# Kernel optimization log

Hardware: AMD Instinct MI355X
Metric: run time of the kernel (lower is better)

## Reference

```python
import jax, jax.numpy as jnp
import numpy as np

B, C, H, W = 4, 320, 32, 32
HEADS = 8
LTXT, DCROSS = 77, 768
HW = H * W


def _ln(x, w, b, eps=1e-5):
    mu = x.mean(-1, keepdims=True)
    var = jnp.var(x, axis=-1, keepdims=True)
    return (x - mu) * jax.lax.rsqrt(var + eps) * w + b


def _gn(x, w, b, groups=32, eps=1e-6):
    Bx, Cx, Hx, Wx = x.shape
    xg = x.reshape(Bx, groups, -1)
    mu = xg.mean(-1, keepdims=True)
    var = jnp.var(xg, axis=-1, keepdims=True)
    xn = ((xg - mu) * jax.lax.rsqrt(var + eps)).reshape(Bx, Cx, Hx, Wx)
    return xn * w[None, :, None, None] + b[None, :, None, None]


def _attn(q, k, v, bias=None):
    Bq, S, Cd = q.shape
    dh = Cd // HEADS
    qh = q.reshape(Bq, S, HEADS, dh)
    kh = k.reshape(Bq, -1, HEADS, dh)
    vh = v.reshape(Bq, -1, HEADS, dh)
    s = jnp.einsum('bqhd,bkhd->bhqk', qh, kh) * (1.0 / np.sqrt(dh))
    if bias is not None:
        s = s + bias  # additive 0/1 otsu mask, exactly as the torch code passes it
    p = jax.nn.softmax(s, axis=-1)
    o = jnp.einsum('bhqk,bkhd->bqhd', p, vh).reshape(Bq, S, Cd)
    return o, p


def _block(x, ctx, prm, bias=None):
    # BasicTransformerBlock: self-attn -> cross-attn (returns probs) -> GEGLU FF
    (ln1w, ln1b, qkv, ow, ob, ln2w, ln2b, q2, kv2, o2w, o2b,
     ln3w, ln3b, ff1w, ff1b, ff2w, ff2b) = prm
    h = _ln(x, ln1w, ln1b)
    q, k, v = jnp.split(h @ qkv, 3, axis=-1)
    o, _ = _attn(q, k, v)
    x = x + o @ ow + ob
    h = _ln(x, ln2w, ln2b)
    k2, v2 = jnp.split(ctx @ kv2, 2, axis=-1)
    o2, p2 = _attn(h @ q2, k2, v2, bias)
    x = x + o2 @ o2w + o2b
    h = _ln(x, ln3w, ln3b)
    a, g = jnp.split(h @ ff1w + ff1b, 2, axis=-1)
    x = x + (a * jax.nn.gelu(g)) @ ff2w + ff2b
    return x, p2


def _otsu(m):
    # vectorized version of the 10-threshold otsu loop (m: [B/2, N])
    mn = m.min(-1, keepdims=True)
    mx = m.max(-1, keepdims=True)
    x = (m - mn) / (mx - mn)
    n = x.shape[-1]
    ts = jnp.arange(10, dtype=x.dtype) * 0.1  # thresholds t*0.1
    low = x[:, None, :] < ts[None, :, None]   # [B/2, 10, N]
    cnt_low = low.sum(-1).astype(x.dtype)
    cnt_high = n - cnt_low
    sum_low = jnp.where(low, x[:, None, :], 0.0).sum(-1)
    sum_high = x.sum(-1, keepdims=True) - sum_low
    mu_low = jnp.where(cnt_low > 0, sum_low / jnp.maximum(cnt_low, 1.0), jnp.nan)
    mu_high = jnp.where(cnt_high > 0, sum_high / jnp.maximum(cnt_high, 1.0), jnp.nan)
    g = (cnt_low / n) * (cnt_high / n) * (mu_low - mu_high) ** 2
    g = jnp.where(jnp.isnan(g), -jnp.inf, g)  # torch: nan > max_g is False -> skipped
    best = jnp.argmax(g, axis=-1)             # first max == torch strict-> ties keep earliest
    gmax = jnp.take_along_axis(g, best[:, None], axis=-1)[:, 0]
    thr = jnp.where(gmax > 0, best.astype(x.dtype) * 0.1, 0.0)[:, None]
    return jnp.where(x < thr, 0.0, jnp.where(x > thr, 1.0, x))


def _fwd(gn_w, gn_b, pin_w, pin_b,
         b_ln1w, b_ln1b, b_qkv, b_ow, b_ob, b_ln2w, b_ln2b, b_q2, b_kv2, b_o2w, b_o2b,
         b_ln3w, b_ln3b, b_ff1w, b_ff1b, b_ff2w, b_ff2b,
         i_ln1w, i_ln1b, i_qkv, i_ow, i_ob, i_ln2w, i_ln2b, i_q2, i_kv2, i_o2w, i_o2b,
         i_ln3w, i_ln3b, i_ff1w, i_ff1b, i_ff2w, i_ff2b,
         pout_w, pout_b, hidden_states, encoder_hidden_states,
         ph_b, ph_t, eot_b, eot_t):
    residual = hidden_states
    h = _gn(hidden_states, gn_w, gn_b)
    h = h.transpose(0, 2, 3, 1).reshape(B, HW, C)
    h = h @ pin_w + pin_b  # use_linear_projection path
    blk = (b_ln1w, b_ln1b, b_qkv, b_ow, b_ob, b_ln2w, b_ln2b, b_q2, b_kv2, b_o2w, b_o2b,
           b_ln3w, b_ln3b, b_ff1w, b_ff1b, b_ff2w, b_ff2b)
    iblk = (i_ln1w, i_ln1b, i_qkv, i_ow, i_ob, i_ln2w, i_ln2b, i_q2, i_kv2, i_o2w, i_o2b,
            i_ln3w, i_ln3b, i_ff1w, i_ff1b, i_ff2w, i_ff2b)
    h, probs = _block(h, encoder_hidden_states, blk)   # probs [B, heads, HW, 77]
    ap = probs.mean(1)[B // 2:]                        # head-avg attn_probs, cond half
    attn = ap.transpose(0, 2, 1)                       # [B/2, 77, HW]
    attn_ph = attn[ph_b, ph_t]                         # [B/2, HW]
    attn_eot = jax.lax.stop_gradient(attn[eot_b, eot_t])
    loss_reg = jnp.mean((attn_ph / attn_ph.max(-1, keepdims=True)
                         - attn_eot / attn_eot.max(-1, keepdims=True)) ** 2)
    mask = _otsu(jax.lax.stop_gradient(attn_ph))       # [B/2, HW]
    bias = mask[:, None, None, :]                      # broadcast over heads and queries
    hs, img = h[:B // 2], h[B // 2:]
    hs, _ = _block(hs, img, iblk, bias)                # image_cross_attention
    h = jnp.concatenate([hs, img], axis=0)
    h = h @ pout_w + pout_b
    sample = h.reshape(B, H, W, C).transpose(0, 3, 1, 2) + residual
    return sample, loss_reg


def setup_inputs():
    key = jax.random.key(0)
    ki = iter(jax.random.split(key, 80))
    f32 = jnp.float32

    def rn(shape, s=0.02):
        return jax.random.normal(next(ki), shape, f32) * s

    def blk(p, cross):
        return {p + 'ln1w': jnp.ones((C,), f32), p + 'ln1b': jnp.zeros((C,), f32),
                p + 'qkv': rn((C, 3 * C)), p + 'ow': rn((C, C)), p + 'ob': jnp.zeros((C,), f32),
                p + 'ln2w': jnp.ones((C,), f32), p + 'ln2b': jnp.zeros((C,), f32),
                p + 'q2': rn((C, C)), p + 'kv2': rn((cross, 2 * C)),
                p + 'o2w': rn((C, C)), p + 'o2b': jnp.zeros((C,), f32),
                p + 'ln3w': jnp.ones((C,), f32), p + 'ln3b': jnp.zeros((C,), f32),
                p + 'ff1w': rn((C, 8 * C)), p + 'ff1b': jnp.zeros((8 * C,), f32),
                p + 'ff2w': rn((4 * C, C)), p + 'ff2b': jnp.zeros((C,), f32)}

    inp = {'gn_w': jnp.ones((C,), f32), 'gn_b': jnp.zeros((C,), f32),
           'pin_w': rn((C, C)), 'pin_b': jnp.zeros((C,), f32)}
    inp.update(blk('b_', DCROSS))
    inp.update(blk('i_', C))
    inp['pout_w'] = rn((C, C))
    inp['pout_b'] = jnp.zeros((C,), f32)
    inp['hidden_states'] = jax.random.normal(next(ki), (B, C, H, W), f32)
    inp['encoder_hidden_states'] = jax.random.normal(next(ki), (B, LTXT, DCROSS), f32)
    inp['ph_b'] = jnp.arange(B // 2)
    inp['ph_t'] = jax.random.randint(next(ki), (B // 2,), 0, LTXT)
    inp['eot_b'] = jnp.arange(B // 2)
    inp['eot_t'] = jax.random.randint(next(ki), (B // 2,), 0, LTXT)
    return inp


def reference(gn_w, gn_b, pin_w, pin_b,
              b_ln1w, b_ln1b, b_qkv, b_ow, b_ob, b_ln2w, b_ln2b, b_q2, b_kv2, b_o2w, b_o2b,
              b_ln3w, b_ln3b, b_ff1w, b_ff1b, b_ff2w, b_ff2b,
              i_ln1w, i_ln1b, i_qkv, i_ow, i_ob, i_ln2w, i_ln2b, i_q2, i_kv2, i_o2w, i_o2b,
              i_ln3w, i_ln3b, i_ff1w, i_ff1b, i_ff2w, i_ff2b,
              pout_w, pout_b, hidden_states, encoder_hidden_states,
              ph_b, ph_t, eot_b, eot_t):
    return _fwd(gn_w, gn_b, pin_w, pin_b,
                b_ln1w, b_ln1b, b_qkv, b_ow, b_ob, b_ln2w, b_ln2b, b_q2, b_kv2, b_o2w, b_o2b,
                b_ln3w, b_ln3b, b_ff1w, b_ff1b, b_ff2w, b_ff2b,
                i_ln1w, i_ln1b, i_qkv, i_ow, i_ob, i_ln2w, i_ln2b, i_q2, i_kv2, i_o2w, i_o2b,
                i_ln3w, i_ln3b, i_ff1w, i_ff1b, i_ff2w, i_ff2b,
                pout_w, pout_b, hidden_states, encoder_hidden_states,
                ph_b, ph_t, eot_b, eot_t)
```

## Files before the change

kernel.cpp:

```cpp
#include <hip/hip_runtime.h>
#include <hip/hip_bf16.h>
#include <math.h>

#define NH 8
#define DH 40
#define CCH 320
#define SCALE 0.15811388300841897f

typedef __attribute__((ext_vector_type(8))) short short8;
typedef __attribute__((ext_vector_type(4))) float float4v;

static __device__ __forceinline__ unsigned short f2bf(float x) {
  __hip_bfloat16 t = __float2bfloat16(x);
  return *reinterpret_cast<unsigned short*>(&t);
}

static __device__ __forceinline__ void gload16(const void* g, void* l) {
  __builtin_amdgcn_global_load_lds((__attribute__((address_space(1))) void*)g,
                                   (__attribute__((address_space(3))) void*)l, 16, 0, 0);
}

__global__ __launch_bounds__(256) void gn_kernel(const float* __restrict__ x,
                                                 const float* __restrict__ w,
                                                 const float* __restrict__ b,
                                                 unsigned short* __restrict__ out) {
  int batch = blockIdx.x >> 5;
  int g = blockIdx.x & 31;
  const int CPG = 10;
  const float* xp = x + ((size_t)batch * CCH + g * CPG) * 1024;
  float s = 0.f, ss = 0.f;
  for (int i = threadIdx.x; i < CPG * 1024; i += 256) { float v = xp[i]; s += v; ss += v * v; }
  __shared__ float r1[256], r2[256];
  r1[threadIdx.x] = s; r2[threadIdx.x] = ss; __syncthreads();
  for (int off = 128; off > 0; off >>= 1) {
    if (threadIdx.x < off) { r1[threadIdx.x] += r1[threadIdx.x + off]; r2[threadIdx.x] += r2[threadIdx.x + off]; }
    __syncthreads();
  }
  float mu = r1[0] * (1.f / 10240.f);
  float var = r2[0] * (1.f / 10240.f) - mu * mu;
  float inv = rsqrtf(var + 1e-6f);
  for (int i = threadIdx.x; i < CPG * 1024; i += 256) {
    int ci = i >> 10; int hw = i & 1023; int c = g * CPG + ci;
    float v = (xp[i] - mu) * inv * w[c] + b[c];
    out[((size_t)batch * 1024 + hw) * CCH + c] = f2bf(v);
  }
}

__global__ __launch_bounds__(256) void ln_kernel(const float* __restrict__ x,
                                                 const float* __restrict__ w,
                                                 const float* __restrict__ b,
                                                 unsigned short* __restrict__ out, int M) {
  int row = blockIdx.x * 4 + (threadIdx.x >> 6);
  if (row >= M) return;
  const float* xp = x + (size_t)row * CCH;
  int lane = threadIdx.x & 63;
  float v[5]; float s = 0.f;
#pragma unroll
  for (int i = 0; i < 5; i++) { v[i] = xp[lane + 64 * i]; s += v[i]; }
#pragma unroll
  for (int o = 32; o > 0; o >>= 1) s += __shfl_xor(s, o);
  float mu = s * (1.f / 320.f);
  float ss = 0.f;
#pragma unroll
  for (int i = 0; i < 5; i++) { float d = v[i] - mu; ss += d * d; }
#pragma unroll
  for (int o = 32; o > 0; o >>= 1) ss += __shfl_xor(ss, o);
  float inv = rsqrtf(ss * (1.f / 320.f) + 1e-5f);
  unsigned short* op = out + (size_t)row * CCH;
#pragma unroll
  for (int i = 0; i < 5; i++) { int c = lane + 64 * i; op[c] = f2bf((v[i] - mu) * inv * w[c] + b[c]); }
}

struct WTab {
  const float* src[16];
  unsigned short* dst[16];
  int Kd[16];
  int Nd[16];
  int perm[16];
  int tstart[17];
  float* lz;
};
__global__ __launch_bounds__(256) void wconv_kernel(WTab t) {
  __shared__ float tile[32][33];
  if (blockIdx.x == 0 && threadIdx.x == 0) *t.lz = 0.f;
  int gid = blockIdx.x;
  int w = 0;
  while (w < 15 && gid >= t.tstart[w + 1]) w++;
  int local = gid - t.tstart[w];
  int K = t.Kd[w], N = t.Nd[w];
  int ntx = (N + 31) >> 5;
  int bx = local % ntx, by = local / ntx;
  int nb = bx * 32, kb = by * 32;
  const float* src = t.src[w];
  unsigned short* dst = t.dst[w];
  int doperm = t.perm[w];
  int half = N >> 1;
  int tx = threadIdx.x & 31, ty = threadIdx.x >> 5;
  for (int i = ty; i < 32; i += 8) {
    int k = kb + i, n = nb + tx;
    tile[i][tx] = (k < K && n < N) ? src[(size_t)k * N + n] : 0.f;
  }
  __syncthreads();
  for (int i = ty; i < 32; i += 8) {
    int n = nb + i, k = kb + tx;
    if (n < N && k < K) {
      int nd = n;
      if (doperm) {
        if (n < half) nd = (n >> 5) * 64 + (n & 31);
        else { int c = n - half; nd = (c >> 5) * 64 + 32 + (c & 31); }
      }
      dst[(size_t)nd * K + k] = f2bf(tile[tx][i]);
    }
  }
}

__global__ __launch_bounds__(256) void mgemm_kernel(const unsigned short* __restrict__ A,
                                                    const unsigned short* __restrict__ Bt,
                                                    const float* __restrict__ bias,
                                                    const float* __restrict__ res,
                                                    void* __restrict__ outp,
                                                    int M, int N, int K, int obf, int gl) {
  __shared__ unsigned short As[128][32];
  __shared__ unsigned short Bs[128][32];
  int tid = threadIdx.x;
  int lane = tid & 63;
  int wave = tid >> 6;
  int wm = (wave & 1) * 64;
  int wn = (wave >> 1) * 64;
  int m0 = blockIdx.y * 128;
  int n0 = blockIdx.x * 128;
  float4v acc[4][4];
  float4v zero = {0.f, 0.f, 0.f, 0.f};
#pragma unroll
  for (int i = 0; i < 4; i++)
#pragma unroll
    for (int j = 0; j < 4; j++) acc[i][j] = zero;
  int fr = lane & 15;
  int kq = (lane >> 4) * 8;
  int c0 = wave * 64 + lane;
  int c1 = c0 + 256;
  const unsigned short* a0 = A + (size_t)(m0 + (c0 >> 2)) * K + (c0 & 3) * 8;
  const unsigned short* a1 = A + (size_t)(m0 + (c1 >> 2)) * K + (c1 & 3) * 8;
  const unsigned short* b0 = Bt + (size_t)(n0 + (c0 >> 2)) * K + (c0 & 3) * 8;
  const unsigned short* b1 = Bt + (size_t)(n0 + (c1 >> 2)) * K + (c1 & 3) * 8;
  char* la0 = ((char*)As) + wave * 1024;
  char* la1 = ((char*)As) + 4096 + wave * 1024;
  char* lb0 = ((char*)Bs) + wave * 1024;
  char* lb1 = ((char*)Bs) + 4096 + wave * 1024;
  for (int k0 = 0; k0 < K; k0 += 32) {
    gload16(a0 + k0, la0);
    gload16(a1 + k0, la1);
    gload16(b0 + k0, lb0);
    gload16(b1 + k0, lb1);
    __syncthreads();
    short8 af[4], bfr[4];
#pragma unroll
    for (int i = 0; i < 4; i++) af[i] = *(short8*)&As[wm + i * 16 + fr][kq];
#pragma unroll
    for (int j = 0; j < 4; j++) bfr[j] = *(short8*)&Bs[wn + j * 16 + fr][kq];
#pragma unroll
    for (int i = 0; i < 4; i++)
#pragma unroll
      for (int j = 0; j < 4; j++)
        acc[i][j] = __builtin_amdgcn_mfma_f32_16x16x32_bf16(af[i], bfr[j], acc[i][j], 0, 0, 0);
    __syncthreads();
  }
  if (gl) {
    int half = N >> 1;
#pragma unroll
    for (int i = 0; i < 4; i++) {
      int mbase = m0 + wm + i * 16 + (lane >> 4) * 4;
#pragma unroll
      for (int jb = 0; jb < 2; jb++) {
        int nout = ((n0 + wn) >> 1) + jb * 16 + (lane & 15);
        float ba = bias[nout];
        float bg = bias[half + nout];
#pragma unroll
        for (int r = 0; r < 4; r++) {
          int m = mbase + r;
          if (m < M) {
            float a = acc[i][jb][r] + ba;
            float g = acc[i][jb + 2][r] + bg;
            float t = tanhf(0.7978845608028654f * (g + 0.044715f * g * g * g));
            ((unsigned short*)outp)[(size_t)m * half + nout] = f2bf(a * (0.5f * g * (1.f + t)));
          }
        }
      }
    }
    return;
  }
#pragma unroll
  for (int i = 0; i < 4; i++) {
    int mbase = m0 + wm + i * 16 + (lane >> 4) * 4;
#pragma unroll
    for (int j = 0; j < 4; j++) {
      int n = n0 + wn + j * 16 + (lane & 15);
      if (n >= N) continue;
      float bv = bias ? bias[n] : 0.f;
#pragma unroll
      for (int r = 0; r < 4; r++) {
        int m = mbase + r;
        if (m < M) {
          float v = acc[i][j][r] + bv;
          if (res) v += res[(size_t)m * N + n];
          if (obf) ((unsigned short*)outp)[(size_t)m * N + n] = f2bf(v);
          else ((float*)outp)[(size_t)m * N + n] = v;
        }
      }
    }
  }
}

__global__ __launch_bounds__(256) void mgemm64_kernel(const void* __restrict__ Ap,
                                                      const unsigned short* __restrict__ Bt,
                                                      const float* __restrict__ bias,
                                                      const float* __restrict__ res,
                                                      void* __restrict__ outp,
                                                      int M, int N, int K, int a32, int omode) {
  __shared__ unsigned short As[64][160];
  __shared__ unsigned short Bs[64][160];
  int tid = threadIdx.x;
  int lane = tid & 63;
  int wv = tid >> 6;
  int quad = lane >> 4;
  int col = lane & 15;
  int m0 = blockIdx.y * 64;
  int n0 = blockIdx.x * 64;
  float4v acc[4];
  float4v zero = {0.f, 0.f, 0.f, 0.f};
#pragma unroll
  for (int j = 0; j < 4; j++) acc[j] = zero;
  short8 vzero = {0, 0, 0, 0, 0, 0, 0, 0};
  int kfast = (!a32) && ((K % 160) == 0);
  int off[5];
#pragma unroll
  for (int i = 0; i < 5; i++) { int c = i * 256 + tid; int row = c / 20; off[i] = row * K + (c - row * 20) * 8; }
  int wb = (tid & 192) * 16;
  const unsigned short* Ab = (const unsigned short*)Ap + (size_t)m0 * K;
  const unsigned short* Bb = Bt + (size_t)n0 * K;
  for (int k0 = 0; k0 < K; k0 += 160) {
    if (kfast) {
#pragma unroll
      for (int i = 0; i < 5; i++) {
        gload16(Ab + off[i] + k0, ((char*)As) + wb + i * 4096);
        gload16(Bb + off[i] + k0, ((char*)Bs) + wb + i * 4096);
      }
    } else {
#pragma unroll
      for (int i = 0; i < 5; i++) {
        int u = tid + i * 256;
        int row = u / 20, seg = u - row * 20;
        int k = k0 + seg * 8;
        int m = m0 + row;
        short8 av = vzero;
        if (m < M && k < K) {
          if (a32) {
            const float* Af = (const float*)Ap;
            float4 f0 = *(const float4*)(Af + (size_t)m * K + k);
            float4 f1 = *(const float4*)(Af + (size_t)m * K + k + 4);
            av[0] = (short)f2bf(f0.x); av[1] = (short)f2bf(f0.y);
            av[2] = (short)f2bf(f0.z); av[3] = (short)f2bf(f0.w);
            av[4] = (short)f2bf(f1.x); av[5] = (short)f2bf(f1.y);
            av[6] = (short)f2bf(f1.z); av[7] = (short)f2bf(f1.w);
          } else {
            av = *(const short8*)((const unsigned short*)Ap + (size_t)m * K + k);
          }
        }
        *(short8*)&As[row][seg * 8] = av;
        int n = n0 + row;
        short8 bv = vzero;
        if (n < N && k < K) bv = *(const short8*)(Bt + (size_t)n * K + k);
        *(short8*)&Bs[row][seg * 8] = bv;
      }
    }
    __syncthreads();
#pragma unroll
    for (int kk = 0; kk < 5; kk++) {
      int kq2 = kk * 32 + quad * 8;
      short8 af = *(short8*)&As[wv * 16 + col][kq2];
#pragma unroll
      for (int j = 0; j < 4; j++) {
        short8 bfr = *(short8*)&Bs[j * 16 + col][kq2];
        acc[j] = __builtin_amdgcn_mfma_f32_16x16x32_bf16(af, bfr, acc[j], 0, 0, 0);
      }
    }
    __syncthreads();
  }
#pragma unroll
  for (int j = 0; j < 4; j++) {
    int n = n0 + j * 16 + col;
    if (n >= N) continue;
    float bv = bias ? bias[n] : 0.f;
#pragma unroll
    for (int r = 0; r < 4; r++) {
      int m = m0 + wv * 16 + quad * 4 + r;
      if (m < M) {
        float v = acc[j][r] + bv;
        if (omode == 2) {
          int bq = m >> 10, hw = m & 1023;
          size_t oi = ((size_t)bq * N + n) * 1024 + hw;
          ((float*)outp)[oi] = v + res[oi];
        } else {
          if (res) v += res[(size_t)m * N + n];
          if (omode == 1) ((unsigned short*)outp)[(size_t)m * N + n] = f2bf(v);
          else ((float*)outp)[(size_t)m * N + n] = v;
        }
      }
    }
  }
}

#define VSTR 72
__global__ __launch_bounds__(256) void mfattn_kernel(const unsigned short* __restrict__ qp, int qstr,
                                                     const unsigned short* __restrict__ kp, int kstr,
                                                     const unsigned short* __restrict__ vp, int vstr,
                                                     const float* __restrict__ bias,
                                                     unsigned short* __restrict__ op) {
  __shared__ unsigned short Ks[64 * 56];
  __shared__ unsigned short Vt[48 * VSTR];
  __shared__ unsigned short Ps[4][16 * 72];
  int tid = threadIdx.x;
  int lane = tid & 63;
  int wv = tid >> 6;
  int quad = lane >> 4;
  int col = lane & 15;
  int bid = blockIdx.x;
  int qt = bid & 15;
  int h = (bid >> 4) & 7;
  int b = bid >> 7;

  short8 zero8 = {0, 0, 0, 0, 0, 0, 0, 0};
  int qrow = qt * 64 + wv * 16 + col;
  const unsigned short* qbase = qp + (size_t)(b * 1024 + qrow) * qstr + h * DH;
  short8 qf0 = *(const short8*)(qbase + quad * 8);
  short8 qf1 = (quad == 0) ? *(const short8*)(qbase + 32) : zero8;

  float4v Oacc[3];
  float4v fzero = {0.f, 0.f, 0.f, 0.f};
  Oacc[0] = fzero; Oacc[1] = fzero; Oacc[2] = fzero;
  float mr[4] = {-3.4e38f, -3.4e38f, -3.4e38f, -3.4e38f};
  float lr[4] = {0.f, 0.f, 0.f, 0.f};

  for (int kt = 0; kt < 16; kt++) {
    int kb = kt * 64;
    __syncthreads();
    for (int u = tid; u < 384; u += 256) {
      int key = u / 6, s = u - key * 6;
      short8 kv8 = zero8;
      if (s < 5) kv8 = *(const short8*)(kp + (size_t)(b * 1024 + kb + key) * kstr + h * DH + s * 8);
      *(short8*)&Ks[key * 56 + s * 8] = kv8;
    }
    for (int u = tid; u < 384; u += 256) {
      int s = u >> 6, key = u & 63;
      short8 vv8 = zero8;
      if (s < 5) vv8 = *(const short8*)(vp + (size_t)(b * 1024 + kb + key) * vstr + h * DH + s * 8);
#pragma unroll
      for (int j = 0; j < 8; j++) Vt[(s * 8 + j) * VSTR + key] = (unsigned short)vv8[j];
    }
    __syncthreads();

    float4v sf[4];
#pragma unroll
    for (int jb = 0; jb < 4; jb++) {
      const unsigned short* krow = &Ks[(jb * 16 + col) * 56];
      short8 bk0 = *(const short8*)(krow + quad * 8);
      short8 bk1 = (quad == 0) ? *(const short8*)(krow + 32) : zero8;
      float4v s = fzero;
      s = __builtin_amdgcn_mfma_f32_16x16x32_bf16(qf0, bk0, s, 0, 0, 0);
      s = __builtin_amdgcn_mfma_f32_16x16x32_bf16(qf1, bk1, s, 0, 0, 0);
      float bv = bias ? bias[b * 1024 + kb + jb * 16 + col] : 0.f;
#pragma unroll
      for (int r = 0; r < 4; r++) s[r] = s[r] * SCALE + bv;
      sf[jb] = s;
    }
    float tmax[4];
#pragma unroll
    for (int r = 0; r < 4; r++) {
      float t = fmaxf(fmaxf(sf[0][r], sf[1][r]), fmaxf(sf[2][r], sf[3][r]));
#pragma unroll
      for (int o = 1; o < 16; o <<= 1) t = fmaxf(t, __shfl_xor(t, o));
      tmax[r] = t;
    }
    float al[4];
#pragma unroll
    for (int r = 0; r < 4; r++) {
      float mnew = fmaxf(mr[r], tmax[r]);
      al[r] = __expf(mr[r] - mnew);
      mr[r] = mnew;
      lr[r] *= al[r];
    }
#pragma unroll
    for (int nb = 0; nb < 3; nb++)
#pragma unroll
      for (int r = 0; r < 4; r++) Oacc[nb][r] *= al[r];
    float rs[4] = {0.f, 0.f, 0.f, 0.f};
#pragma unroll
    for (int jb = 0; jb < 4; jb++) {
#pragma unroll
      for (int r = 0; r < 4; r++) {
        float p = __expf(sf[jb][r] - mr[r]);
        rs[r] += p;
        Ps[wv][(quad * 4 + r) * 72 + jb * 16 + col] = f2bf(p);
      }
    }
#pragma unroll
    for (int r = 0; r < 4; r++) {
      float t = rs[r];
#pragma unroll
      for (int o = 1; o < 16; o <<= 1) t += __shfl_xor(t, o);
      lr[r] += t;
    }
#pragma unroll
    for (int kc = 0; kc < 2; kc++) {
      int koff = kc * 32 + quad * 8;
      short8 pa = *(const short8*)&Ps[wv][col * 72 + koff];
#pragma unroll
      for (int nb = 0; nb < 3; nb++) {
        short8 vb = *(const short8*)&Vt[(nb * 16 + col) * VSTR + koff];
        Oacc[nb] = __builtin_amdgcn_mfma_f32_16x16x32_bf16(pa, vb, Oacc[nb], 0, 0, 0);
      }
    }
  }
#pragma unroll
  for (int r = 0; r < 4; r++) {
    int qo = qt * 64 + wv * 16 + quad * 4 + r;
    float invl = 1.f / lr[r];
    unsigned short* orow = op + (size_t)(b * 1024 + qo) * CCH + h * DH;
#pragma unroll
    for (int nb = 0; nb < 3; nb++) {
      int d = nb * 16 + col;
      if (d < DH) orow[d] = f2bf(Oacc[nb][r] * invl);
    }
  }
}

#define CVSTR 104
__global__ __launch_bounds__(256) void cattnm_kernel(const unsigned short* __restrict__ qp,
                                                     const unsigned short* __restrict__ kvp,
                                                     unsigned short* __restrict__ op,
                                                     float* __restrict__ probs) {
  __shared__ unsigned short Ks[80 * 56];
  __shared__ unsigned short Vt[48 * CVSTR];
  __shared__ unsigned short Ps[4][16 * 104];
  int tid = threadIdx.x;
  int lane = tid & 63;
  int wv = tid >> 6;
  int quad = lane >> 4;
  int col = lane & 15;
  int bid = blockIdx.x;
  int qt = bid & 15;
  int h = (bid >> 4) & 7;
  int b = bid >> 7;

  short8 zero8 = {0, 0, 0, 0, 0, 0, 0, 0};
  for (int u = tid; u < 480; u += 256) {
    int key = u / 6, s = u - key * 6;
    short8 v8 = zero8;
    if (s < 5 && key < 77) v8 = *(const short8*)(kvp + (size_t)(b * 77 + key) * 640 + h * DH + s * 8);
    *(short8*)&Ks[key * 56 + s * 8] = v8;
  }
  for (int u = tid; u < 576; u += 256) {
    int s = u / 96, key = u - s * 96;
    short8 v8 = zero8;
    if (s < 5 && key < 77) v8 = *(const short8*)(kvp + (size_t)(b * 77 + key) * 640 + 320 + h * DH + s * 8);
#pragma unroll
    for (int j = 0; j < 8; j++) Vt[(s * 8 + j) * CVSTR + key] = (unsigned short)v8[j];
  }
  int qrow = qt * 64 + wv * 16 + col;
  const unsigned short* qbase = qp + (size_t)(b * 1024 + qrow) * CCH + h * DH;
  short8 qf0 = *(const short8*)(qbase + quad * 8);
  short8 qf1 = (quad == 0) ? *(const short8*)(qbase + 32) : zero8;
  __syncthreads();

  float4v fzero = {0.f, 0.f, 0.f, 0.f};
  float4v sf[5];
#pragma unroll
  for (int jb = 0; jb < 5; jb++) {
    const unsigned short* krow = &Ks[(jb * 16 + col) * 56];
    short8 bk0 = *(const short8*)(krow + quad * 8);
    short8 bk1 = (quad == 0) ? *(const short8*)(krow + 32) : zero8;
    float4v s = fzero;
    s = __builtin_amdgcn_mfma_f32_16x16x32_bf16(qf0, bk0, s, 0, 0, 0);
    s = __builtin_amdgcn_mfma_f32_16x16x32_bf16(qf1, bk1, s, 0, 0, 0);
    int key = jb * 16 + col;
    float msk = (key < 77) ? 0.f : -3.4e38f;
#pragma unroll
    for (int r = 0; r < 4; r++) s[r] = s[r] * SCALE + msk;
    sf[jb] = s;
  }
  float inv[4];
#pragma unroll
  for (int r = 0; r < 4; r++) {
    float t = sf[0][r];
#pragma unroll
    for (int jb = 1; jb < 5; jb++) t = fmaxf(t, sf[jb][r]);
#pragma unroll
    for (int o = 1; o < 16; o <<= 1) t = fmaxf(t, __shfl_xor(t, o));
    float sum = 0.f;
#pragma unroll
    for (int jb = 0; jb < 5; jb++) { float e = __expf(sf[jb][r] - t); sf[jb][r] = e; sum += e; }
#pragma unroll
    for (int o = 1; o < 16; o <<= 1) sum += __shfl_xor(sum, o);
    inv[r] = 1.f / sum;
  }
#pragma unroll
  for (int jb = 0; jb < 5; jb++) {
    int key = jb * 16 + col;
    float4v pv;
#pragma unroll
    for (int r = 0; r < 4; r++) {
      float p = sf[jb][r] * inv[r];
      Ps[wv][(quad * 4 + r) * 104 + jb * 16 + col] = f2bf(p);
      pv[r] = p;
    }
    if (b >= 2 && key < 77) {
      size_t pi = ((size_t)((b - 2) * NH + h) * 77 + key) * 1024 + qt * 64 + wv * 16 + quad * 4;
      *(float4v*)&probs[pi] = pv;
    }
  }
  float4v Oacc[3];
  Oacc[0] = fzero; Oacc[1] = fzero; Oacc[2] = fzero;
#pragma unroll
  for (int kc = 0; kc < 3; kc++) {
    int koff = kc * 32 + quad * 8;
    short8 pa = (koff < 80) ? *(const short8*)&Ps[wv][col * 104 + koff] : zero8;
#pragma unroll
    for (int nb = 0; nb < 3; nb++) {
      short8 vb = *(const short8*)&Vt[(nb * 16 + col) * CVSTR + koff];
      Oacc[nb] = __builtin_amdgcn_mfma_f32_16x16x32_bf16(pa, vb, Oacc[nb], 0, 0, 0);
    }
  }
#pragma unroll
  for (int r = 0; r < 4; r++) {
    int qo = qt * 64 + wv * 16 + quad * 4 + r;
    unsigned short* orow = op + (size_t)(b * 1024 + qo) * CCH + h * DH;
#pragma unroll
    for (int nb = 0; nb < 3; nb++) {
      int d = nb * 16 + col;
      if (d < DH) orow[d] = f2bf(Oacc[nb][r]);
    }
  }
}

__global__ __launch_bounds__(256) void eol_kernel(const float* __restrict__ pT,
                                                  const int* __restrict__ phb, const int* __restrict__ pht,
                                                  const int* __restrict__ eob, const int* __restrict__ eot,
                                                  float* __restrict__ mask,
                                                  float* __restrict__ lossout) {
  __shared__ float S[4][24];
  __shared__ float shthr;
  int i = blockIdx.x, tid = threadIdx.x;
  int lane = tid & 63, wv = tid >> 6;
  int pb = phb[i], pt = pht[i], eb = eob[i], et = eot[i];
  float x[4], y[4];
#pragma unroll
  for (int j = 0; j < 4; j++) {
    int q = tid + 256 * j;
    float s1 = 0.f, s2 = 0.f;
#pragma unroll
    for (int hh = 0; hh < NH; hh++) {
      s1 += pT[((size_t)(pb * NH + hh) * 77 + pt) * 1024 + q];
      s2 += pT[((size_t)(eb * NH + hh) * 77 + et) * 1024 + q];
    }
    x[j] = s1 * 0.125f;
    y[j] = s2 * 0.125f;
  }
  float mx = fmaxf(fmaxf(x[0], x[1]), fmaxf(x[2], x[3]));
  float me = fmaxf(fmaxf(y[0], y[1]), fmaxf(y[2], y[3]));
  float mn = fminf(fminf(x[0], x[1]), fminf(x[2], x[3]));
  float sx = x[0] + x[1] + x[2] + x[3];
#pragma unroll
  for (int o = 32; o > 0; o >>= 1) {
    mx = fmaxf(mx, __shfl_xor(mx, o));
    me = fmaxf(me, __shfl_xor(me, o));
    mn = fminf(mn, __shfl_xor(mn, o));
    sx += __shfl_xor(sx, o);
  }
  if (lane == 0) { S[wv][0] = mx; S[wv][1] = me; S[wv][2] = mn; S[wv][3] = sx; }
  __syncthreads();
  mx = fmaxf(fmaxf(S[0][0], S[1][0]), fmaxf(S[2][0], S[3][0]));
  me = fmaxf(fmaxf(S[0][1], S[1][1]), fmaxf(S[2][1], S[3][1]));
  mn = fminf(fminf(S[0][2], S[1][2]), fminf(S[2][2], S[3][2]));
  sx = S[0][3] + S[1][3] + S[2][3] + S[3][3];
  float invmp = 1.f / mx, invme = 1.f / me;
  float inv = 1.f / (mx - mn);
  float lp = 0.f;
  float cnt[10], sm[10];
#pragma unroll
  for (int t = 0; t < 10; t++) { cnt[t] = 0.f; sm[t] = 0.f; }
#pragma unroll
  for (int j = 0; j < 4; j++) {
    float d = x[j] * invmp - y[j] * invme;
    lp += d * d;
    float v = (x[j] - mn) * inv;
#pragma unroll
    for (int t = 0; t < 10; t++) {
      if (v < t * 0.1f) { cnt[t] += 1.f; sm[t] += v; }
    }
  }
#pragma unroll
  for (int o = 32; o > 0; o >>= 1) {
    lp += __shfl_xor(lp, o);
#pragma unroll
    for (int t = 0; t < 10; t++) { cnt[t] += __shfl_xor(cnt[t], o); sm[t] += __shfl_xor(sm[t], o); }
  }
  __syncthreads();
  if (lane == 0) {
    S[wv][0] = lp;
#pragma unroll
    for (int t = 0; t < 10; t++) { S[wv][1 + t] = cnt[t]; S[wv][11 + t] = sm[t]; }
  }
  __syncthreads();
  if (tid == 0) {
    float lpt = S[0][0] + S[1][0] + S[2][0] + S[3][0];
    atomicAdd(lossout, lpt * (1.f / 2048.f));
    float total = (sx - 1024.f * mn) * inv;
    float gmax = -3.4e38f; int best = 0;
    for (int t = 0; t < 10; t++) {
      float c_low = S[0][1 + t] + S[1][1 + t] + S[2][1 + t] + S[3][1 + t];
      float s_low = S[0][11 + t] + S[1][11 + t] + S[2][11 + t] + S[3][11 + t];
      float c_high = 1024.f - c_low;
      float g;
      if (c_low > 0.f && c_high > 0.f) {
        float mu_l = s_low / c_low;
        float mu_h = (total - s_low) / c_high;
        float dd = mu_l - mu_h;
        g = (c_low * (1.f / 1024.f)) * (c_high * (1.f / 1024.f)) * dd * dd;
      } else g = -3.4e38f;
      if (g > gmax) { gmax = g; best = t; }
    }
    shthr = (gmax > 0.f) ? best * 0.1f : 0.f;
  }
  __syncthreads();
  float thr = shthr;
#pragma unroll
  for (int j = 0; j < 4; j++) {
    int q = tid + 256 * j;
    float v = (x[j] - mn) * inv;
    mask[i * 1024 + q] = (v < thr) ? 0.f : ((v > thr) ? 1.f : v);
  }
}

extern "C" void kernel_launch(void* const* d_in, const int* in_sizes, int n_in,
                              void* d_out, int out_size, void* d_ws, size_t ws_size,
                              hipStream_t stream) {
  auto F = [&](int i) { return (const float*)d_in[i]; };
  auto I = [&](int i) { return (const int*)d_in[i]; };

  float* ws = (float*)d_ws;
  float* h    = ws;
  float* ffb  = h    + 1310720;
  float* p2   = ffb  + 10485760;
  float* mask = p2   + 2523136;

  unsigned short* b16   = (unsigned short*)(mask + 2048);
  unsigned short* lnb16 = b16;
  unsigned short* attb16= lnb16 + 1310720;
  unsigned short* actb16= attb16 + 1310720;
  unsigned short* qkv16 = actb16 + 5242880;
  unsigned short* q16   = qkv16 + 3932160;
  unsigned short* kv16  = q16 + 1310720;
  unsigned short* wptr  = kv16 + 1310720;

  auto walloc = [&](int n) { unsigned short* p = wptr; wptr += n; return p; };
  unsigned short* pin_t  = walloc(102400);
  unsigned short* bqkv_t = walloc(307200);
  unsigned short* bow_t  = walloc(102400);
  unsigned short* bq2_t  = walloc(102400);
  unsigned short* bkv2_t = walloc(491520);
  unsigned short* bo2_t  = walloc(102400);
  unsigned short* bff1_t = walloc(819200);
  unsigned short* bff2_t = walloc(409600);
  unsigned short* iqkv_t = walloc(307200);
  unsigned short* iow_t  = walloc(102400);
  unsigned short* iq2_t  = walloc(102400);
  unsigned short* ikv2_t = walloc(204800);
  unsigned short* io2_t  = walloc(102400);
  unsigned short* iff1_t = walloc(819200);
  unsigned short* iff2_t = walloc(409600);
  unsigned short* pout_t = walloc(102400);

  float* out = (float*)d_out;

  WTab wt;
  wt.lz = out + 1310720;
  int nt = 0, cnt = 0;
  auto addw = [&](const float* s, unsigned short* d, int K, int N, int perm) {
    wt.src[cnt] = s; wt.dst[cnt] = d; wt.Kd[cnt] = K; wt.Nd[cnt] = N; wt.perm[cnt] = perm;
    wt.tstart[cnt] = nt;
    nt += ((K + 31) / 32) * ((N + 31) / 32);
    cnt++;
  };
  addw(F(2), pin_t, 320, 320, 0);
  addw(F(4 + 2), bqkv_t, 320, 960, 0);
  addw(F(4 + 3), bow_t, 320, 320, 0);
  addw(F(4 + 7), bq2_t, 320, 320, 0);
  addw(F(4 + 8), bkv2_t, 768, 640, 0);
  addw(F(4 + 9), bo2_t, 320, 320, 0);
  addw(F(4 + 13), bff1_t, 320, 2560, 1);
  addw(F(4 + 15), bff2_t, 1280, 320, 0);
  addw(F(21 + 2), iqkv_t, 320, 960, 0);
  addw(F(21 + 3), iow_t, 320, 320, 0);
  addw(F(21 + 7), iq2_t, 320, 320, 0);
  addw(F(21 + 8), ikv2_t, 320, 640, 0);
  addw(F(21 + 9), io2_t, 320, 320, 0);
  addw(F(21 + 13), iff1_t, 320, 2560, 1);
  addw(F(21 + 15), iff2_t, 1280, 320, 0);
  addw(F(38), pout_t, 320, 320, 0);
  wt.tstart[16] = nt;

  wconv_kernel<<<nt, 256, 0, stream>>>(wt);

  auto gemm64 = [&](const void* A, const unsigned short* Wt, const float* bias,
                    const float* res, void* o, int M, int N, int K, int a32, int omode) {
    dim3 g((N + 63) / 64, (M + 63) / 64);
    mgemm64_kernel<<<g, 256, 0, stream>>>(A, Wt, bias, res, o, M, N, K, a32, omode);
  };
  auto gemm128 = [&](const unsigned short* A, const unsigned short* Wt, const float* bias,
                     const float* res, void* o, int M, int N, int K, int obf, int gl) {
    dim3 g((N + 127) / 128, (M + 127) / 128);
    mgemm_kernel<<<g, 256, 0, stream>>>(A, Wt, bias, res, o, M, N, K, obf, gl);
  };

  gn_kernel<<<128, 256, 0, stream>>>(F(40), F(0), F(1), lnb16);
  gemm64(lnb16, pin_t, F(3), nullptr, h, 4096, 320, 320, 0, 0);

  auto run_block = [&](int p, int Bx, bool img_block,
                       const unsigned short* qkv_t, const unsigned short* ow_t,
                       const unsigned short* q2_t, const unsigned short* kv2_t,
                       const unsigned short* o2_t, const unsigned short* ff1_t,
                       const unsigned short* ff2_t) {
    int M = Bx * 1024;
    ln_kernel<<<M / 4, 256, 0, stream>>>(h, F(p + 0), F(p + 1), lnb16, M);
    gemm128(lnb16, qkv_t, nullptr, nullptr, qkv16, M, 960, 320, 1, 0);
    mfattn_kernel<<<Bx * 128, 256, 0, stream>>>(qkv16, 960, qkv16 + 320, 960, qkv16 + 640, 960,
                                                nullptr, attb16);
    gemm64(attb16, ow_t, F(p + 4), h, h, M, 320, 320, 0, 0);
    ln_kernel<<<M / 4, 256, 0, stream>>>(h, F(p + 5), F(p + 6), lnb16, M);
    if (!img_block) {
      gemm64(F(41), kv2_t, nullptr, nullptr, kv16, Bx * 77, 640, 768, 1, 1);
      gemm64(lnb16, q2_t, nullptr, nullptr, q16, M, 320, 320, 0, 1);
      cattnm_kernel<<<Bx * 128, 256, 0, stream>>>(q16, kv16, attb16, p2);
    } else {
      gemm64(h + (size_t)2 * 1024 * 320, kv2_t, nullptr, nullptr, kv16, Bx * 1024, 640, 320, 1, 1);
      gemm64(lnb16, q2_t, nullptr, nullptr, q16, M, 320, 320, 0, 1);
      mfattn_kernel<<<Bx * 128, 256, 0, stream>>>(q16, 320, kv16, 640, kv16 + 320, 640,
                                                  mask, attb16);
    }
    gemm64(attb16, o2_t, F(p + 10), h, h, M, 320, 320, 0, 0);
    ln_kernel<<<M / 4, 256, 0, stream>>>(h, F(p + 11), F(p + 12), lnb16, M);
    gemm128(lnb16, ff1_t, F(p + 14), nullptr, actb16, M, 2560, 320, 1, 1);
    gemm64(actb16, ff2_t, F(p + 16), h, h, M, 320, 1280, 0, 0);
  };

  run_block(4, 4, false, bqkv_t, bow_t, bq2_t, bkv2_t, bo2_t, bff1_t, bff2_t);

  eol_kernel<<<2, 256, 0, stream>>>(p2, I(42), I(43), I(44), I(45), mask, out + 1310720);

  run_block(21, 2, true, iqkv_t, iow_t, iq2_t, ikv2_t, io2_t, iff1_t, iff2_t);

  gemm64(h, pout_t, F(39), F(40), out, 4096, 320, 320, 1, 2);
}
```

Before: 591.3 us.

## Split-K flash attention into four key chunks with a separate merge kernel

The self-attention and image cross-attention kernels now split the 1024 keys into four chunks, launching four times as many blocks. Each block writes unnormalized fp32 partial outputs plus row max and sum to scratch, and a new merge kernel rescales, combines and writes bf16 output. The goal is more parallelism and better occupancy on a GPU with many CUs, since before only 256 or 512 blocks were launched. The cost is extra global traffic for the fp32 partials and one more kernel launch per attention call.

```diff
diff --git a/kernel.cpp b/kernel.cpp
--- a/kernel.cpp
+++ b/kernel.cpp
@@ -311,11 +311,13 @@
 }
 
 #define VSTR 72
-__global__ __launch_bounds__(256) void mfattn_kernel(const unsigned short* __restrict__ qp, int qstr,
-                                                     const unsigned short* __restrict__ kp, int kstr,
-                                                     const unsigned short* __restrict__ vp, int vstr,
-                                                     const float* __restrict__ bias,
-                                                     unsigned short* __restrict__ op) {
+__global__ __launch_bounds__(256) void mfattns_kernel(const unsigned short* __restrict__ qp, int qstr,
+                                                      const unsigned short* __restrict__ kp, int kstr,
+                                                      const unsigned short* __restrict__ vp, int vstr,
+                                                      const float* __restrict__ bias,
+                                                      float* __restrict__ Opart,
+                                                      float* __restrict__ mpart,
+                                                      float* __restrict__ lpart) {
   __shared__ unsigned short Ks[64 * 56];
   __shared__ unsigned short Vt[48 * VSTR];
   __shared__ unsigned short Ps[4][16 * 72];
@@ -325,9 +327,10 @@
   int quad = lane >> 4;
   int col = lane & 15;
   int bid = blockIdx.x;
-  int qt = bid & 15;
-  int h = (bid >> 4) & 7;
-  int b = bid >> 7;
+  int split = bid & 3;
+  int qt = (bid >> 2) & 15;
+  int h = (bid >> 6) & 7;
+  int b = bid >> 9;
 
   short8 zero8 = {0, 0, 0, 0, 0, 0, 0, 0};
   int qrow = qt * 64 + wv * 16 + col;
@@ -341,7 +344,7 @@
   float mr[4] = {-3.4e38f, -3.4e38f, -3.4e38f, -3.4e38f};
   float lr[4] = {0.f, 0.f, 0.f, 0.f};
 
-  for (int kt = 0; kt < 16; kt++) {
+  for (int kt = split * 4; kt < split * 4 + 4; kt++) {
     int kb = kt * 64;
     __syncthreads();
     for (int u = tid; u < 384; u += 256) {
@@ -424,13 +427,49 @@
 #pragma unroll
   for (int r = 0; r < 4; r++) {
     int qo = qt * 64 + wv * 16 + quad * 4 + r;
-    float invl = 1.f / lr[r];
-    unsigned short* orow = op + (size_t)(b * 1024 + qo) * CCH + h * DH;
+    size_t rowidx = (size_t)(b * NH + h) * 1024 + qo;
+    float* orow = Opart + (rowidx * 4 + split) * DH;
 #pragma unroll
     for (int nb = 0; nb < 3; nb++) {
       int d = nb * 16 + col;
-      if (d < DH) orow[d] = f2bf(Oacc[nb][r] * invl);
-    }
+      if (d < DH) orow[d] = Oacc[nb][r];
+    }
+    if (col == 0) {
+      mpart[rowidx * 4 + split] = mr[r];
+      lpart[rowidx * 4 + split] = lr[r];
+    }
+  }
+}
+
+__global__ __launch_bounds__(256) void merge_kernel(const float* __restrict__ Opart,
+                                                    const float* __restrict__ mpart,
+                                                    const float* __restrict__ lpart,
+                                                    unsigned short* __restrict__ op, int rows) {
+  int r = blockIdx.x * 256 + threadIdx.x;
+  if (r >= rows) return;
+  float m0 = mpart[r * 4 + 0], m1 = mpart[r * 4 + 1], m2 = mpart[r * 4 + 2], m3 = mpart[r * 4 + 3];
+  float M = fmaxf(fmaxf(m0, m1), fmaxf(m2, m3));
+  float w0 = __expf(m0 - M), w1 = __expf(m1 - M), w2 = __expf(m2 - M), w3 = __expf(m3 - M);
+  float L = lpart[r * 4 + 0] * w0 + lpart[r * 4 + 1] * w1 + lpart[r * 4 + 2] * w2 + lpart[r * 4 + 3] * w3;
+  float inv = 1.f / L;
+  w0 *= inv; w1 *= inv; w2 *= inv; w3 *= inv;
+  int q = r & 1023;
+  int h = (r >> 10) & 7;
+  int b = r >> 13;
+  const float4* p0 = (const float4*)(Opart + (size_t)(r * 4 + 0) * DH);
+  const float4* p1 = (const float4*)(Opart + (size_t)(r * 4 + 1) * DH);
+  const float4* p2 = (const float4*)(Opart + (size_t)(r * 4 + 2) * DH);
+  const float4* p3 = (const float4*)(Opart + (size_t)(r * 4 + 3) * DH);
+  unsigned short* o = op + ((size_t)(b * 1024 + q)) * 320 + h * DH;
+#pragma unroll
+  for (int j = 0; j < 10; j++) {
+    float4 a = p0[j], bb = p1[j], c = p2[j], d = p3[j];
+    ushort4 pk;
+    pk.x = f2bf(a.x * w0 + bb.x * w1 + c.x * w2 + d.x * w3);
+    pk.y = f2bf(a.y * w0 + bb.y * w1 + c.y * w2 + d.y * w3);
+    pk.z = f2bf(a.z * w0 + bb.z * w1 + c.z * w2 + d.z * w3);
+    pk.w = f2bf(a.w * w0 + bb.w * w1 + c.w * w2 + d.w * w3);
+    *(ushort4*)(o + j * 4) = pk;
   }
 }
 
@@ -652,6 +691,10 @@
   float* ffb  = h    + 1310720;
   float* p2   = ffb  + 10485760;
   float* mask = p2   + 2523136;
+
+  float* Opart = ffb;
+  float* mpart = ffb + 5242880;
+  float* lpart = ffb + 5242880 + 131072;
 
   unsigned short* b16   = (unsigned short*)(mask + 2048);
   unsigned short* lnb16 = b16;
@@ -733,8 +776,9 @@
     int M = Bx * 1024;
     ln_kernel<<<M / 4, 256, 0, stream>>>(h, F(p + 0), F(p + 1), lnb16, M);
     gemm128(lnb16, qkv_t, nullptr, nullptr, qkv16, M, 960, 320, 1, 0);
-    mfattn_kernel<<<Bx * 128, 256, 0, stream>>>(qkv16, 960, qkv16 + 320, 960, qkv16 + 640, 960,
-                                                nullptr, attb16);
+    mfattns_kernel<<<Bx * 512, 256, 0, stream>>>(qkv16, 960, qkv16 + 320, 960, qkv16 + 640, 960,
+                                                 nullptr, Opart, mpart, lpart);
+    merge_kernel<<<Bx * 32, 256, 0, stream>>>(Opart, mpart, lpart, attb16, Bx * 8192);
     gemm64(attb16, ow_t, F(p + 4), h, h, M, 320, 320, 0, 0);
     ln_kernel<<<M / 4, 256, 0, stream>>>(h, F(p + 5), F(p + 6), lnb16, M);
     if (!img_block) {
@@ -744,8 +788,9 @@
     } else {
       gemm64(h + (size_t)2 * 1024 * 320, kv2_t, nullptr, nullptr, kv16, Bx * 1024, 640, 320, 1, 1);
       gemm64(lnb16, q2_t, nullptr, nullptr, q16, M, 320, 320, 0, 1);
-      mfattn_kernel<<<Bx * 128, 256, 0, stream>>>(q16, 320, kv16, 640, kv16 + 320, 640,
-                                                  mask, attb16);
+      mfattns_kernel<<<Bx * 512, 256, 0, stream>>>(q16, 320, kv16, 640, kv16 + 320, 640,
+                                                   mask, Opart, mpart, lpart);
+      merge_kernel<<<Bx * 32, 256, 0, stream>>>(Opart, mpart, lpart, attb16, Bx * 8192);
     }
     gemm64(attb16, o2_t, F(p + 10), h, h, M, 320, 320, 0, 0);
     ln_kernel<<<M / 4, 256, 0, stream>>>(h, F(p + 11), F(p + 12), lnb16, M);
```

New measurement: 579.3 us. 1.02x faster.
